# Kernel tuning notes

Measured on AMD Instinct MI355X. Metric: run time of the kernel, lower is better.

## Reference

```python
import jax, jax.numpy as jnp
import numpy as np

V, BLK, D, H, L = 32000, 2048, 768, 12, 2
HD = D // H

def _ln(x, g, b, eps=1e-5):
    m = jnp.mean(x, axis=-1, keepdims=True)
    v = jnp.var(x, axis=-1, keepdims=True)
    return (x - m) * jax.lax.rsqrt(v + eps) * g + b

def setup_inputs() -> dict:
    key = jax.random.key(0)
    ks = jax.random.split(key, 16)
    s = 0.02
    return {
        "idx": jax.random.randint(ks[0], (2, 2048), 0, V, dtype=jnp.int32),
        "wte": jax.random.normal(ks[1], (V, D), jnp.float32) * s,
        "wpe": jax.random.normal(ks[2], (BLK, D), jnp.float32) * s,
        "ln1_g": jnp.ones((L, D), jnp.float32),
        "ln1_b": jnp.zeros((L, D), jnp.float32),
        "qkv_w": jax.random.normal(ks[3], (L, 3 * D, D), jnp.float32) * s,
        "qkv_b": jnp.zeros((L, 3 * D), jnp.float32),
        "proj_w": jax.random.normal(ks[4], (L, D, D), jnp.float32) * s,
        "proj_b": jnp.zeros((L, D), jnp.float32),
        "ln2_g": jnp.ones((L, D), jnp.float32),
        "ln2_b": jnp.zeros((L, D), jnp.float32),
        "fc_w": jax.random.normal(ks[5], (L, 4 * D, D), jnp.float32) * s,
        "fc_b": jnp.zeros((L, 4 * D), jnp.float32),
        "fc2_w": jax.random.normal(ks[6], (L, D, 4 * D), jnp.float32) * s,
        "fc2_b": jnp.zeros((L, D), jnp.float32),
        "lnf_g": jnp.ones((D,), jnp.float32),
        "lnf_b": jnp.zeros((D,), jnp.float32),
    }

def reference(idx, wte, wpe, ln1_g, ln1_b, qkv_w, qkv_b, proj_w, proj_b,
              ln2_g, ln2_b, fc_w, fc_b, fc2_w, fc2_b, lnf_g, lnf_b):
    B, T = idx.shape
    x = wte[idx] + wpe[:T][None, :, :]  # [B,T,D]
    causal = jnp.tril(jnp.ones((T, T), dtype=bool))
    scale = 1.0 / np.sqrt(HD)
    for l in range(L):
        h = _ln(x, ln1_g[l], ln1_b[l])
        qkv = h @ qkv_w[l].T + qkv_b[l]               # [B,T,3D]
        q, k, v = jnp.split(qkv, 3, axis=-1)
        q = q.reshape(B, T, H, HD).transpose(0, 2, 1, 3)
        k = k.reshape(B, T, H, HD).transpose(0, 2, 1, 3)
        v = v.reshape(B, T, H, HD).transpose(0, 2, 1, 3)
        att = jnp.einsum('bhqd,bhkd->bhqk', q, k) * scale
        att = jnp.where(causal, att, -jnp.inf)
        att = jax.nn.softmax(att, axis=-1)
        y = jnp.einsum('bhqk,bhkd->bhqd', att, v)
        y = y.transpose(0, 2, 1, 3).reshape(B, T, D)
        x = x + y @ proj_w[l].T + proj_b[l]
        h = _ln(x, ln2_g[l], ln2_b[l])
        h = jax.nn.gelu(h @ fc_w[l].T + fc_b[l], approximate=False)
        x = x + h @ fc2_w[l].T + fc2_b[l]
    x = _ln(x, lnf_g, lnf_b)
    logits = x @ wte.T  # tied lm_head, [B,T,V]
    return logits
```

## Files before the change

kernel.cpp:

```cpp
#include <hip/hip_runtime.h>
#include <hip/hip_bf16.h>
#include <math.h>

#define BB 2
#define TT 2048
#define DD 768
#define HH 12
#define NTOK (BB*TT)
#define VV 32000
#define NL 2

typedef __hip_bfloat16 bf16;
typedef __attribute__((ext_vector_type(8))) short bf16x8;
typedef __attribute__((ext_vector_type(4))) float f32x4;

typedef const __attribute__((address_space(1))) unsigned int* gas_u32;
typedef __attribute__((address_space(3))) unsigned int* las_u32;

__device__ __forceinline__ void gload16(const bf16* g, bf16* l) {
    __builtin_amdgcn_global_load_lds((gas_u32)g, (las_u32)l, 16, 0, 0);
}

__global__ void cast_f2b(const float* __restrict__ in, bf16* __restrict__ out, int n4) {
    int i = blockIdx.x * 256 + threadIdx.x;
    if (i >= n4) return;
    float4 v = reinterpret_cast<const float4*>(in)[i];
    out[i*4+0] = __float2bfloat16(v.x);
    out[i*4+1] = __float2bfloat16(v.y);
    out[i*4+2] = __float2bfloat16(v.z);
    out[i*4+3] = __float2bfloat16(v.w);
}

__global__ void embed_k(const int* __restrict__ idx, const float* __restrict__ wte,
                        const float* __restrict__ wpe, float* __restrict__ x) {
    int i = blockIdx.x * 256 + threadIdx.x;
    int n = i / (DD/4), d4 = i - n * (DD/4);
    int tok = idx[n];
    int t = n & (TT - 1);
    float4 a = reinterpret_cast<const float4*>(wte + (size_t)tok * DD)[d4];
    float4 p = reinterpret_cast<const float4*>(wpe + (size_t)t * DD)[d4];
    float4 r; r.x = a.x+p.x; r.y = a.y+p.y; r.z = a.z+p.z; r.w = a.w+p.w;
    reinterpret_cast<float4*>(x)[i] = r;
}

__global__ __launch_bounds__(256) void ln_k(const float* __restrict__ x,
                                            const float* __restrict__ g,
                                            const float* __restrict__ b,
                                            bf16* __restrict__ out) {
    int row = blockIdx.x;
    int tid = threadIdx.x;
    const float* xr = x + (size_t)row * DD;
    float v0 = xr[tid], v1 = xr[tid + 256], v2 = xr[tid + 512];
    float s = v0 + v1 + v2;
    float ss = v0*v0 + v1*v1 + v2*v2;
    #pragma unroll
    for (int d = 1; d < 64; d <<= 1) { s += __shfl_xor(s, d, 64); ss += __shfl_xor(ss, d, 64); }
    __shared__ float sh[8];
    int w = tid >> 6;
    if ((tid & 63) == 0) { sh[w] = s; sh[4 + w] = ss; }
    __syncthreads();
    s  = sh[0] + sh[1] + sh[2] + sh[3];
    ss = sh[4] + sh[5] + sh[6] + sh[7];
    float mean = s * (1.0f / DD);
    float var  = ss * (1.0f / DD) - mean * mean;
    float rstd = rsqrtf(var + 1e-5f);
    bf16* orow = out + (size_t)row * DD;
    orow[tid]       = __float2bfloat16((v0 - mean) * rstd * g[tid]       + b[tid]);
    orow[tid + 256] = __float2bfloat16((v1 - mean) * rstd * g[tid + 256] + b[tid + 256]);
    orow[tid + 512] = __float2bfloat16((v2 - mean) * rstd * g[tid + 512] + b[tid + 512]);
}

template<int EPI, bool SWZ>
__global__ __launch_bounds__(512, 1) void gemm256(
    const bf16* __restrict__ A, const bf16* __restrict__ W,
    const float* __restrict__ bias, const float* __restrict__ resid,
    void* __restrict__ outp, int O, int K, int nwgx)
{
    __shared__ bf16 smem_bf[65536];
    char* smem = (char*)smem_bf;
    const int tid = threadIdx.x, lane = tid & 63, wid = tid >> 6;
    const int wm = wid >> 2, wn = wid & 3;
    int f = blockIdx.x;
    if (SWZ) { int x = f & 7, r = f >> 3; f = x * ((int)gridDim.x >> 3) + r; }
    const int by = f / nwgx;
    const int bx = f - by * nwgx;
    const int rowBase = by * 256, colBase = bx * 256;
    const int rr = lane & 15, s4 = lane >> 4;
    const int swz = (rr >> 1) & 3;
    const int aOff = (wm * 128 + rr) * 64 + ((s4 ^ swz) << 4);
    const int bOff = (wn * 64 + rr) * 64 + ((s4 ^ swz) << 4);
    const int st_r = (wid << 4) + (lane >> 2);
    const int st_j = lane & 3;
    const bf16* Asrc = A + (size_t)rowBase * K;
    const bf16* Wsrc = W + (size_t)colBase * K;
    const int nk = K >> 6;

    auto STAGE = [&](const bf16* src, int mat, int kt, int kk) {
        char* base = smem + ((kt & 1) << 16) + (mat << 15) + (kk << 14);
        #pragma unroll
        for (int L = 0; L < 2; ++L) {
            int r = (L << 7) + st_r;
            int gs = st_j ^ ((r >> 1) & 3);
            gload16(src + (size_t)r * K + (kt << 6) + (kk << 5) + (gs << 3),
                    (bf16*)(base + (L << 13) + (wid << 10)));
        }
    };

    f32x4 acc[8][4];
    #pragma unroll
    for (int m = 0; m < 8; ++m)
        #pragma unroll
        for (int n = 0; n < 4; ++n) acc[m][n] = (f32x4){0.f, 0.f, 0.f, 0.f};

    STAGE(Asrc, 0, 0, 0); STAGE(Wsrc, 1, 0, 0); STAGE(Asrc, 0, 0, 1); STAGE(Wsrc, 1, 0, 1);
    STAGE(Asrc, 0, 1, 0); STAGE(Wsrc, 1, 1, 0); STAGE(Asrc, 0, 1, 1);
    asm volatile("s_waitcnt vmcnt(6)" ::: "memory");
    __builtin_amdgcn_s_barrier();

    bf16x8 af[8], bfr[2];
    for (int kt = 0; kt < nk; ++kt) {
        char* Ab = smem + ((kt & 1) << 16);
        char* Bb = Ab + 32768;
        #pragma unroll
        for (int q = 0; q < 4; ++q) {
            const int kk = q >> 1, nh = q & 1;
            if (nh == 0) {
                #pragma unroll
                for (int m = 0; m < 8; ++m)
                    af[m] = *reinterpret_cast<const bf16x8*>(Ab + (kk << 14) + aOff + (m << 10));
            }
            bfr[0] = *reinterpret_cast<const bf16x8*>(Bb + (kk << 14) + bOff + ((nh * 2 + 0) << 10));
            bfr[1] = *reinterpret_cast<const bf16x8*>(Bb + (kk << 14) + bOff + ((nh * 2 + 1) << 10));
            if (q == 0) { if (kt + 1 < nk) STAGE(Wsrc, 1, kt + 1, 1); }
            else if (q == 1) { if (kt + 2 < nk) STAGE(Asrc, 0, kt + 2, 0); }
            else if (q == 2) { if (kt + 2 < nk) STAGE(Wsrc, 1, kt + 2, 0); }
            else { if (kt + 2 < nk) STAGE(Asrc, 0, kt + 2, 1); }
            __builtin_amdgcn_s_barrier();
            __builtin_amdgcn_s_setprio(1);
            #pragma unroll
            for (int m = 0; m < 8; ++m) {
                acc[m][nh * 2 + 0] = __builtin_amdgcn_mfma_f32_16x16x32_bf16(af[m], bfr[0], acc[m][nh * 2 + 0], 0, 0, 0);
                acc[m][nh * 2 + 1] = __builtin_amdgcn_mfma_f32_16x16x32_bf16(af[m], bfr[1], acc[m][nh * 2 + 1], 0, 0, 0);
            }
            __builtin_amdgcn_s_setprio(0);
            if (q == 3) asm volatile("s_waitcnt vmcnt(6)" ::: "memory");
            __builtin_amdgcn_s_barrier();
        }
    }

    #pragma unroll
    for (int m = 0; m < 8; ++m) {
        int row = rowBase + wm * 128 + m * 16 + s4 * 4;
        #pragma unroll
        for (int n = 0; n < 4; ++n) {
            int col = colBase + wn * 64 + n * 16 + rr;
            float bv = bias ? bias[col] : 0.f;
            #pragma unroll
            for (int j2 = 0; j2 < 4; ++j2) {
                float v = acc[m][n][j2] + bv;
                size_t oi = (size_t)(row + j2) * O + col;
                if (EPI == 1) v += resid[oi];
                if (EPI == 2) {
                    v = 0.5f * v * (1.0f + erff(v * 0.70710678118654752f));
                    reinterpret_cast<bf16*>(outp)[oi] = __float2bfloat16(v);
                } else if (EPI == 3) {
                    reinterpret_cast<bf16*>(outp)[oi] = __float2bfloat16(v);
                } else {
                    reinterpret_cast<float*>(outp)[oi] = v;
                }
            }
        }
    }
}

template<int EPI>
__global__ __launch_bounds__(256) void gemm_bt(
    const bf16* __restrict__ A, const bf16* __restrict__ W,
    const float* __restrict__ bias, const float* __restrict__ resid,
    void* __restrict__ outp, int O, int K)
{
    __shared__ bf16 As[128 * 32];
    __shared__ bf16 Bs[128 * 32];
    const int tid = threadIdx.x;
    const int lane = tid & 63;
    const int w = tid >> 6;
    const int wm = w >> 1, wn = w & 1;
    const int rowBase = blockIdx.y * 128, colBase = blockIdx.x * 128;

    const int rr = lane & 15, kq = (lane >> 4) * 8;
    const int srow = lane >> 2;
    const int scol = (lane & 3) * 8;

    f32x4 acc[4][4];
    #pragma unroll
    for (int m = 0; m < 4; ++m)
        #pragma unroll
        for (int n = 0; n < 4; ++n) acc[m][n] = (f32x4){0.f, 0.f, 0.f, 0.f};

    for (int k0 = 0; k0 < K; k0 += 32) {
        #pragma unroll
        for (int p = 0; p < 2; ++p) {
            int s = w * 16 + p * 64;
            gload16(&A[(size_t)(rowBase + s + srow) * K + k0 + scol], &As[s * 32]);
            gload16(&W[(size_t)(colBase + s + srow) * K + k0 + scol], &Bs[s * 32]);
        }
        __syncthreads();
        bf16x8 a[4], b[4];
        #pragma unroll
        for (int m = 0; m < 4; ++m)
            a[m] = *reinterpret_cast<const bf16x8*>(&As[(wm * 64 + m * 16 + rr) * 32 + kq]);
        #pragma unroll
        for (int n = 0; n < 4; ++n)
            b[n] = *reinterpret_cast<const bf16x8*>(&Bs[(wn * 64 + n * 16 + rr) * 32 + kq]);
        #pragma unroll
        for (int m = 0; m < 4; ++m)
            #pragma unroll
            for (int n = 0; n < 4; ++n)
                acc[m][n] = __builtin_amdgcn_mfma_f32_16x16x32_bf16(a[m], b[n], acc[m][n], 0, 0, 0);
        __syncthreads();
    }

    #pragma unroll
    for (int m = 0; m < 4; ++m) {
        int row = rowBase + wm * 64 + m * 16 + (lane >> 4) * 4;
        #pragma unroll
        for (int n = 0; n < 4; ++n) {
            int col = colBase + wn * 64 + n * 16 + (lane & 15);
            float bv = bias ? bias[col] : 0.f;
            #pragma unroll
            for (int j2 = 0; j2 < 4; ++j2) {
                float v = acc[m][n][j2] + bv;
                size_t oi = (size_t)(row + j2) * O + col;
                if (EPI == 1) v += resid[oi];
                if (EPI == 2) {
                    v = 0.5f * v * (1.0f + erff(v * 0.70710678118654752f));
                    reinterpret_cast<bf16*>(outp)[oi] = __float2bfloat16(v);
                } else if (EPI == 3) {
                    reinterpret_cast<bf16*>(outp)[oi] = __float2bfloat16(v);
                } else {
                    reinterpret_cast<float*>(outp)[oi] = v;
                }
            }
        }
    }
}

__global__ __launch_bounds__(256, 2) void attn_flash(const bf16* __restrict__ qkvb,
                                                     bf16* __restrict__ ybf)
{
    __shared__ bf16 Qs[128][72];
    __shared__ bf16 Ks[64][72];
    __shared__ bf16 Vt[64][72];

    const int tid = threadIdx.x, lane = tid & 63, w = tid >> 6;
    const int qi = 15 - (blockIdx.x / 24);
    const int bh = blockIdx.x % 24;
    const int b = bh / HH, h = bh % HH;
    const int qbase = qi * 128;
    const int rr = lane & 15, g8 = (lane >> 4) * 8, g4 = (lane >> 4) * 4;

    {
        int seg = tid & 7, jr = tid >> 3;
        #pragma unroll
        for (int p = 0; p < 4; ++p) {
            int q = jr + p * 32;
            *reinterpret_cast<uint4*>(&Qs[q][seg * 8]) =
                *reinterpret_cast<const uint4*>(&qkvb[(size_t)(b*TT + qbase + q) * 2304 + h*64 + seg*8]);
        }
    }
    __syncthreads();

    bf16x8 qf[2][2];
    #pragma unroll
    for (int m = 0; m < 2; ++m)
        #pragma unroll
        for (int c = 0; c < 2; ++c)
            qf[m][c] = *reinterpret_cast<const bf16x8*>(&Qs[w*32 + m*16 + rr][c*32 + g8]);

    float mst[2][4], lst[2][4];
    f32x4 o[2][4];
    #pragma unroll
    for (int m = 0; m < 2; ++m)
        #pragma unroll
        for (int jj = 0; jj < 4; ++jj) { mst[m][jj] = -1e30f; lst[m][jj] = 0.f; }
    #pragma unroll
    for (int m = 0; m < 2; ++m)
        #pragma unroll
        for (int nd = 0; nd < 4; ++nd) o[m][nd] = (f32x4){0.f,0.f,0.f,0.f};

    const int ktmax = 2 * qi + 2;
    for (int kt = 0; kt < ktmax; ++kt) {
        __syncthreads();
        {
            int seg = tid & 7, jr = tid >> 3;
            #pragma unroll
            for (int p = 0; p < 2; ++p) {
                int j = jr + p * 32;
                *reinterpret_cast<uint4*>(&Ks[j][seg * 8]) =
                    *reinterpret_cast<const uint4*>(&qkvb[(size_t)(b*TT + kt*64 + j) * 2304 + DD + h*64 + seg*8]);
            }
            int jv = tid & 31, d0 = (tid >> 5) * 8;
            #pragma unroll
            for (int p = 0; p < 2; ++p) {
                int j = jv + p * 32;
                uint4 raw = *reinterpret_cast<const uint4*>(&qkvb[(size_t)(b*TT + kt*64 + j) * 2304 + 2*DD + h*64 + d0]);
                const bf16* vv = reinterpret_cast<const bf16*>(&raw);
                #pragma unroll
                for (int i2 = 0; i2 < 8; ++i2) Vt[d0 + i2][j] = vv[i2];
            }
        }
        __syncthreads();

        bf16x8 kf[4][2];
        #pragma unroll
        for (int n = 0; n < 4; ++n)
            #pragma unroll
            for (int c = 0; c < 2; ++c)
                kf[n][c] = *reinterpret_cast<const bf16x8*>(&Ks[n*16 + rr][c*32 + g8]);
        f32x4 sacc[2][4];
        #pragma unroll
        for (int m = 0; m < 2; ++m)
            #pragma unroll
            for (int n = 0; n < 4; ++n) sacc[m][n] = (f32x4){0.f,0.f,0.f,0.f};
        #pragma unroll
        for (int m = 0; m < 2; ++m)
            #pragma unroll
            for (int n = 0; n < 4; ++n)
                #pragma unroll
                for (int c = 0; c < 2; ++c)
                    sacc[m][n] = __builtin_amdgcn_mfma_f32_16x16x32_bf16(qf[m][c], kf[n][c], sacc[m][n], 0, 0, 0);

        float corr[2][4];
        #pragma unroll
        for (int m = 0; m < 2; ++m) {
            #pragma unroll
            for (int jj = 0; jj < 4; ++jj) {
                const int qg = qbase + w*32 + m*16 + g4 + jj;
                float pm = -1e30f;
                #pragma unroll
                for (int n = 0; n < 4; ++n) {
                    float v = sacc[m][n][jj] * 0.125f;
                    int jg = kt*64 + n*16 + rr;
                    v = (jg <= qg) ? v : -1e30f;
                    sacc[m][n][jj] = v;
                    pm = fmaxf(pm, v);
                }
                pm = fmaxf(pm, __shfl_xor(pm, 1, 64));
                pm = fmaxf(pm, __shfl_xor(pm, 2, 64));
                pm = fmaxf(pm, __shfl_xor(pm, 4, 64));
                pm = fmaxf(pm, __shfl_xor(pm, 8, 64));
                float nm = fmaxf(mst[m][jj], pm);
                float cv = __expf(mst[m][jj] - nm);
                float r = 0.f;
                #pragma unroll
                for (int n = 0; n < 4; ++n) {
                    float p = __expf(sacc[m][n][jj] - nm);
                    r += p;
                    Qs[w*32 + m*16 + g4 + jj][n*16 + rr] = __float2bfloat16(p);
                }
                r += __shfl_xor(r, 1, 64);
                r += __shfl_xor(r, 2, 64);
                r += __shfl_xor(r, 4, 64);
                r += __shfl_xor(r, 8, 64);
                lst[m][jj] = lst[m][jj] * cv + r;
                mst[m][jj] = nm;
                corr[m][jj] = cv;
            }
        }
        #pragma unroll
        for (int m = 0; m < 2; ++m)
            #pragma unroll
            for (int nd = 0; nd < 4; ++nd)
                #pragma unroll
                for (int jj = 0; jj < 4; ++jj) o[m][nd][jj] *= corr[m][jj];

        __builtin_amdgcn_sched_barrier(0);

        bf16x8 pf[2][2], vf[4][2];
        #pragma unroll
        for (int m = 0; m < 2; ++m)
            #pragma unroll
            for (int c = 0; c < 2; ++c)
                pf[m][c] = *reinterpret_cast<const bf16x8*>(&Qs[w*32 + m*16 + rr][c*32 + g8]);
        #pragma unroll
        for (int nd = 0; nd < 4; ++nd)
            #pragma unroll
            for (int c = 0; c < 2; ++c)
                vf[nd][c] = *reinterpret_cast<const bf16x8*>(&Vt[nd*16 + rr][c*32 + g8]);
        #pragma unroll
        for (int m = 0; m < 2; ++m)
            #pragma unroll
            for (int nd = 0; nd < 4; ++nd)
                #pragma unroll
                for (int c = 0; c < 2; ++c)
                    o[m][nd] = __builtin_amdgcn_mfma_f32_16x16x32_bf16(pf[m][c], vf[nd][c], o[m][nd], 0, 0, 0);
    }

    #pragma unroll
    for (int m = 0; m < 2; ++m) {
        #pragma unroll
        for (int jj = 0; jj < 4; ++jj) {
            const int qg = qbase + w*32 + m*16 + g4 + jj;
            const float inv = 1.0f / lst[m][jj];
            #pragma unroll
            for (int nd = 0; nd < 4; ++nd)
                ybf[(size_t)(b*TT + qg) * DD + h*64 + nd*16 + rr] =
                    __float2bfloat16(o[m][nd][jj] * inv);
        }
    }
}

extern "C" void kernel_launch(void* const* d_in, const int* in_sizes, int n_in,
                              void* d_out, int out_size, void* d_ws, size_t ws_size,
                              hipStream_t stream) {
    const int*   idx    = (const int*)  d_in[0];
    const float* wte    = (const float*)d_in[1];
    const float* wpe    = (const float*)d_in[2];
    const float* ln1_g  = (const float*)d_in[3];
    const float* ln1_b  = (const float*)d_in[4];
    const float* qkv_w  = (const float*)d_in[5];
    const float* qkv_b  = (const float*)d_in[6];
    const float* proj_w = (const float*)d_in[7];
    const float* proj_b = (const float*)d_in[8];
    const float* ln2_g  = (const float*)d_in[9];
    const float* ln2_b  = (const float*)d_in[10];
    const float* fc_w   = (const float*)d_in[11];
    const float* fc_b   = (const float*)d_in[12];
    const float* fc2_w  = (const float*)d_in[13];
    const float* fc2_b  = (const float*)d_in[14];
    const float* lnf_g  = (const float*)d_in[15];
    const float* lnf_b  = (const float*)d_in[16];

    char* ws = (char*)d_ws;
    size_t off = 0;
    auto alloc = [&](size_t bytes) -> void* {
        void* p = ws + off;
        off += (bytes + 255) & ~(size_t)255;
        return p;
    };
    float* x     = (float*)alloc((size_t)NTOK * DD * 4);
    bf16*  qkvb  = (bf16*) alloc((size_t)NTOK * 3 * DD * 2);
    bf16*  lnb   = (bf16*) alloc((size_t)NTOK * DD * 2);
    bf16*  ybf   = (bf16*) alloc((size_t)NTOK * DD * 2);
    bf16*  ffb   = (bf16*) alloc((size_t)NTOK * 4 * DD * 2);
    bf16*  w_qkv = (bf16*) alloc((size_t)NL * 3 * DD * DD * 2);
    bf16*  w_prj = (bf16*) alloc((size_t)NL * DD * DD * 2);
    bf16*  w_fc  = (bf16*) alloc((size_t)NL * 4 * DD * DD * 2);
    bf16*  w_fc2 = (bf16*) alloc((size_t)NL * DD * 4 * DD * 2);
    bf16*  w_wte = (bf16*) alloc((size_t)VV * DD * 2);

    auto conv = [&](const float* src, bf16* dst, size_t n) {
        int n4 = (int)(n / 4);
        cast_f2b<<<dim3((n4 + 255) / 256), dim3(256), 0, stream>>>(src, dst, n4);
    };
    conv(wte,    w_wte, (size_t)VV * DD);
    conv(qkv_w,  w_qkv, (size_t)NL * 3 * DD * DD);
    conv(proj_w, w_prj, (size_t)NL * DD * DD);
    conv(fc_w,   w_fc,  (size_t)NL * 4 * DD * DD);
    conv(fc2_w,  w_fc2, (size_t)NL * DD * 4 * DD);

    embed_k<<<dim3(NTOK * (DD/4) / 256), dim3(256), 0, stream>>>(idx, wte, wpe, x);

    for (int l = 0; l < NL; ++l) {
        ln_k<<<dim3(NTOK), dim3(256), 0, stream>>>(x, ln1_g + l * DD, ln1_b + l * DD, lnb);
        gemm_bt<3><<<dim3(3 * DD / 128, 32), dim3(256), 0, stream>>>(
            lnb, w_qkv + (size_t)l * 3 * DD * DD, qkv_b + l * 3 * DD, nullptr,
            (void*)qkvb, 3 * DD, DD);
        attn_flash<<<dim3(24 * (TT / 128)), dim3(256), 0, stream>>>(qkvb, ybf);
        gemm_bt<1><<<dim3(DD / 128, 32), dim3(256), 0, stream>>>(
            ybf, w_prj + (size_t)l * DD * DD, proj_b + l * DD, x,
            (void*)x, DD, DD);
        ln_k<<<dim3(NTOK), dim3(256), 0, stream>>>(x, ln2_g + l * DD, ln2_b + l * DD, lnb);
        gemm_bt<2><<<dim3(4 * DD / 128, 32), dim3(256), 0, stream>>>(
            lnb, w_fc + (size_t)l * 4 * DD * DD, fc_b + l * 4 * DD, nullptr,
            (void*)ffb, 4 * DD, DD);
        gemm_bt<1><<<dim3(DD / 128, 32), dim3(256), 0, stream>>>(
            ffb, w_fc2 + (size_t)l * DD * 4 * DD, fc2_b + l * DD, x,
            (void*)x, DD, 4 * DD);
    }

    ln_k<<<dim3(NTOK), dim3(256), 0, stream>>>(x, lnf_g, lnf_b, lnb);
    gemm256<0, true><<<dim3((VV / 256) * (NTOK / 256)), dim3(512), 0, stream>>>(
        lnb, w_wte, nullptr, nullptr, d_out, VV, DD, VV / 256);
}
```

Before: 884.2 us.

## Prefetch next K/V tile into registers in attention, skip masks, remap lm_head tiles

The flash attention loop now loads the next K/V tile from global memory into registers while the current tile is being computed, and stores it to LDS at the start of the next iteration. This hides global load latency behind the MFMA work. Causal masking is skipped for sub-tiles that lie entirely below the diagonal, and s_setprio is raised around the MFMA blocks. The lm_head GEMM also switches to a new block-to-tile mapping that groups 16 row tiles across 8 XCD-strided slots, which changes cache locality.

```diff
diff --git a/kernel.cpp b/kernel.cpp
--- a/kernel.cpp
+++ b/kernel.cpp
@@ -70,7 +70,7 @@
     orow[tid + 512] = __float2bfloat16((v2 - mean) * rstd * g[tid + 512] + b[tid + 512]);
 }
 
-template<int EPI, bool SWZ>
+template<int EPI, int SWZMODE>
 __global__ __launch_bounds__(512, 1) void gemm256(
     const bf16* __restrict__ A, const bf16* __restrict__ W,
     const float* __restrict__ bias, const float* __restrict__ resid,
@@ -81,9 +81,14 @@
     const int tid = threadIdx.x, lane = tid & 63, wid = tid >> 6;
     const int wm = wid >> 2, wn = wid & 3;
     int f = blockIdx.x;
-    if (SWZ) { int x = f & 7, r = f >> 3; f = x * ((int)gridDim.x >> 3) + r; }
-    const int by = f / nwgx;
-    const int bx = f - by * nwgx;
+    int by, bx;
+    if (SWZMODE == 2) {
+        int x = f & 7, r = f >> 3;
+        by = x * 2 + (r & 1);
+        bx = r >> 1;
+    } else {
+        by = f / nwgx; bx = f - by * nwgx;
+    }
     const int rowBase = by * 256, colBase = bx * 256;
     const int rr = lane & 15, s4 = lane >> 4;
     const int swz = (rr >> 1) & 3;
@@ -268,6 +273,20 @@
                 *reinterpret_cast<const uint4*>(&qkvb[(size_t)(b*TT + qbase + q) * 2304 + h*64 + seg*8]);
         }
     }
+
+    const int seg = tid & 7, jr = tid >> 3;
+    const int jv = tid & 31, d0 = (tid >> 5) * 8;
+    const bf16* kbase = qkvb + (size_t)b * TT * 2304 + DD + h * 64;
+    const bf16* vbase = qkvb + (size_t)b * TT * 2304 + 2 * DD + h * 64;
+    uint4 kreg[2], vreg[2];
+    auto LOADKV = [&](int kt) {
+        #pragma unroll
+        for (int p = 0; p < 2; ++p) {
+            kreg[p] = *reinterpret_cast<const uint4*>(&kbase[(size_t)(kt*64 + jr + p*32) * 2304 + seg*8]);
+            vreg[p] = *reinterpret_cast<const uint4*>(&vbase[(size_t)(kt*64 + jv + p*32) * 2304 + d0]);
+        }
+    };
+    LOADKV(0);
     __syncthreads();
 
     bf16x8 qf[2][2];
@@ -290,26 +309,17 @@
 
     const int ktmax = 2 * qi + 2;
     for (int kt = 0; kt < ktmax; ++kt) {
-        __syncthreads();
-        {
-            int seg = tid & 7, jr = tid >> 3;
-            #pragma unroll
-            for (int p = 0; p < 2; ++p) {
-                int j = jr + p * 32;
-                *reinterpret_cast<uint4*>(&Ks[j][seg * 8]) =
-                    *reinterpret_cast<const uint4*>(&qkvb[(size_t)(b*TT + kt*64 + j) * 2304 + DD + h*64 + seg*8]);
-            }
-            int jv = tid & 31, d0 = (tid >> 5) * 8;
-            #pragma unroll
-            for (int p = 0; p < 2; ++p) {
-                int j = jv + p * 32;
-                uint4 raw = *reinterpret_cast<const uint4*>(&qkvb[(size_t)(b*TT + kt*64 + j) * 2304 + 2*DD + h*64 + d0]);
-                const bf16* vv = reinterpret_cast<const bf16*>(&raw);
-                #pragma unroll
-                for (int i2 = 0; i2 < 8; ++i2) Vt[d0 + i2][j] = vv[i2];
-            }
-        }
-        __syncthreads();
+        #pragma unroll
+        for (int p = 0; p < 2; ++p) {
+            *reinterpret_cast<uint4*>(&Ks[jr + p*32][seg*8]) = kreg[p];
+            const bf16* vv = reinterpret_cast<const bf16*>(&vreg[p]);
+            #pragma unroll
+            for (int i2 = 0; i2 < 8; ++i2) Vt[d0 + i2][jv + p*32] = vv[i2];
+        }
+        if (kt + 1 < ktmax) LOADKV(kt + 1);
+        asm volatile("s_waitcnt lgkmcnt(0)" ::: "memory");
+        __builtin_amdgcn_s_barrier();
+        __builtin_amdgcn_sched_barrier(0);
 
         bf16x8 kf[4][2];
         #pragma unroll
@@ -322,6 +332,7 @@
         for (int m = 0; m < 2; ++m)
             #pragma unroll
             for (int n = 0; n < 4; ++n) sacc[m][n] = (f32x4){0.f,0.f,0.f,0.f};
+        __builtin_amdgcn_s_setprio(1);
         #pragma unroll
         for (int m = 0; m < 2; ++m)
             #pragma unroll
@@ -329,10 +340,12 @@
                 #pragma unroll
                 for (int c = 0; c < 2; ++c)
                     sacc[m][n] = __builtin_amdgcn_mfma_f32_16x16x32_bf16(qf[m][c], kf[n][c], sacc[m][n], 0, 0, 0);
+        __builtin_amdgcn_s_setprio(0);
 
         float corr[2][4];
         #pragma unroll
         for (int m = 0; m < 2; ++m) {
+            const bool needMask = (kt*64 + 63) > (qbase + w*32 + m*16);
             #pragma unroll
             for (int jj = 0; jj < 4; ++jj) {
                 const int qg = qbase + w*32 + m*16 + g4 + jj;
@@ -340,8 +353,10 @@
                 #pragma unroll
                 for (int n = 0; n < 4; ++n) {
                     float v = sacc[m][n][jj] * 0.125f;
-                    int jg = kt*64 + n*16 + rr;
-                    v = (jg <= qg) ? v : -1e30f;
+                    if (needMask) {
+                        int jg = kt*64 + n*16 + rr;
+                        v = (jg <= qg) ? v : -1e30f;
+                    }
                     sacc[m][n][jj] = v;
                     pm = fmaxf(pm, v);
                 }
@@ -387,6 +402,7 @@
             #pragma unroll
             for (int c = 0; c < 2; ++c)
                 vf[nd][c] = *reinterpret_cast<const bf16x8*>(&Vt[nd*16 + rr][c*32 + g8]);
+        __builtin_amdgcn_s_setprio(1);
         #pragma unroll
         for (int m = 0; m < 2; ++m)
             #pragma unroll
@@ -394,6 +410,9 @@
                 #pragma unroll
                 for (int c = 0; c < 2; ++c)
                     o[m][nd] = __builtin_amdgcn_mfma_f32_16x16x32_bf16(pf[m][c], vf[nd][c], o[m][nd], 0, 0, 0);
+        __builtin_amdgcn_s_setprio(0);
+
+        __builtin_amdgcn_s_barrier();
     }
 
     #pragma unroll
@@ -480,6 +499,6 @@
     }
 
     ln_k<<<dim3(NTOK), dim3(256), 0, stream>>>(x, lnf_g, lnf_b, lnb);
-    gemm256<0, true><<<dim3((VV / 256) * (NTOK / 256)), dim3(512), 0, stream>>>(
+    gemm256<0, 2><<<dim3((VV / 256) * (NTOK / 256)), dim3(512), 0, stream>>>(
         lnb, w_wte, nullptr, nullptr, d_out, VV, DD, VV / 256);
 }
```

New measurement: 917.0 us. +3.7%, slower.

## Fold softmax scale into Q, use exp2, skip rescale and masking when unneeded

Applied to the files above, without the earlier changes.

Pre-multiplies Q by scale·log2(e) so the softmax can use exp2f without a per-element scale. It skips causal masking on KV tiles that are fully below the diagonal. It also skips the running-max update and output rescale when the new row max exceeds the old one by at most 8 in log2 units (lazy rescaling). MFMA sections are wrapped in s_setprio to favour matrix issue. The risks are bf16 rounding of the pre-scaled Q and the possibility that lazy rescaling lets values grow up to 2^8 before normalisation. The GEMM swizzle template parameter is renamed without changing behaviour.

```diff
diff --git a/kernel.cpp b/kernel.cpp
--- a/kernel.cpp
+++ b/kernel.cpp
@@ -19,6 +19,13 @@
 
 __device__ __forceinline__ void gload16(const bf16* g, bf16* l) {
     __builtin_amdgcn_global_load_lds((gas_u32)g, (las_u32)l, 16, 0, 0);
+}
+__device__ __forceinline__ float b2f(short s) {
+    union { float f; unsigned u; } x; x.u = ((unsigned)(unsigned short)s) << 16; return x.f;
+}
+__device__ __forceinline__ short f2b(float f) {
+    __hip_bfloat16 h = __float2bfloat16(f);
+    return *reinterpret_cast<short*>(&h);
 }
 
 __global__ void cast_f2b(const float* __restrict__ in, bf16* __restrict__ out, int n4) {
@@ -70,7 +77,7 @@
     orow[tid + 512] = __float2bfloat16((v2 - mean) * rstd * g[tid + 512] + b[tid + 512]);
 }
 
-template<int EPI, bool SWZ>
+template<int EPI, int SWZMODE>
 __global__ __launch_bounds__(512, 1) void gemm256(
     const bf16* __restrict__ A, const bf16* __restrict__ W,
     const float* __restrict__ bias, const float* __restrict__ resid,
@@ -81,7 +88,7 @@
     const int tid = threadIdx.x, lane = tid & 63, wid = tid >> 6;
     const int wm = wid >> 2, wn = wid & 3;
     int f = blockIdx.x;
-    if (SWZ) { int x = f & 7, r = f >> 3; f = x * ((int)gridDim.x >> 3) + r; }
+    if (SWZMODE == 1) { int x = f & 7, r = f >> 3; f = x * ((int)gridDim.x >> 3) + r; }
     const int by = f / nwgx;
     const int bx = f - by * nwgx;
     const int rowBase = by * 256, colBase = bx * 256;
@@ -274,8 +281,12 @@
     #pragma unroll
     for (int m = 0; m < 2; ++m)
         #pragma unroll
-        for (int c = 0; c < 2; ++c)
-            qf[m][c] = *reinterpret_cast<const bf16x8*>(&Qs[w*32 + m*16 + rr][c*32 + g8]);
+        for (int c = 0; c < 2; ++c) {
+            bf16x8 v = *reinterpret_cast<const bf16x8*>(&Qs[w*32 + m*16 + rr][c*32 + g8]);
+            #pragma unroll
+            for (int e = 0; e < 8; ++e) v[e] = f2b(b2f(v[e]) * 0.180336880111f);
+            qf[m][c] = v;
+        }
 
     float mst[2][4], lst[2][4];
     f32x4 o[2][4];
@@ -322,6 +333,7 @@
         for (int m = 0; m < 2; ++m)
             #pragma unroll
             for (int n = 0; n < 4; ++n) sacc[m][n] = (f32x4){0.f,0.f,0.f,0.f};
+        __builtin_amdgcn_s_setprio(1);
         #pragma unroll
         for (int m = 0; m < 2; ++m)
             #pragma unroll
@@ -329,50 +341,85 @@
                 #pragma unroll
                 for (int c = 0; c < 2; ++c)
                     sacc[m][n] = __builtin_amdgcn_mfma_f32_16x16x32_bf16(qf[m][c], kf[n][c], sacc[m][n], 0, 0, 0);
-
-        float corr[2][4];
+        __builtin_amdgcn_s_setprio(0);
+
+        float pm[2][4];
+        float need = -1e30f;
         #pragma unroll
         for (int m = 0; m < 2; ++m) {
+            const bool needMask = (kt*64 + 63) > (qbase + w*32 + m*16);
             #pragma unroll
             for (int jj = 0; jj < 4; ++jj) {
                 const int qg = qbase + w*32 + m*16 + g4 + jj;
-                float pm = -1e30f;
+                float pv = -1e30f;
                 #pragma unroll
                 for (int n = 0; n < 4; ++n) {
-                    float v = sacc[m][n][jj] * 0.125f;
-                    int jg = kt*64 + n*16 + rr;
-                    v = (jg <= qg) ? v : -1e30f;
-                    sacc[m][n][jj] = v;
-                    pm = fmaxf(pm, v);
+                    float v = sacc[m][n][jj];
+                    if (needMask) {
+                        int jg = kt*64 + n*16 + rr;
+                        v = (jg <= qg) ? v : -1e30f;
+                        sacc[m][n][jj] = v;
+                    }
+                    pv = fmaxf(pv, v);
                 }
-                pm = fmaxf(pm, __shfl_xor(pm, 1, 64));
-                pm = fmaxf(pm, __shfl_xor(pm, 2, 64));
-                pm = fmaxf(pm, __shfl_xor(pm, 4, 64));
-                pm = fmaxf(pm, __shfl_xor(pm, 8, 64));
-                float nm = fmaxf(mst[m][jj], pm);
-                float cv = __expf(mst[m][jj] - nm);
-                float r = 0.f;
-                #pragma unroll
-                for (int n = 0; n < 4; ++n) {
-                    float p = __expf(sacc[m][n][jj] - nm);
-                    r += p;
-                    Qs[w*32 + m*16 + g4 + jj][n*16 + rr] = __float2bfloat16(p);
+                pv = fmaxf(pv, __shfl_xor(pv, 1, 64));
+                pv = fmaxf(pv, __shfl_xor(pv, 2, 64));
+                pv = fmaxf(pv, __shfl_xor(pv, 4, 64));
+                pv = fmaxf(pv, __shfl_xor(pv, 8, 64));
+                pm[m][jj] = pv;
+                need = fmaxf(need, pv - mst[m][jj]);
+            }
+        }
+
+        if (__all(need <= 8.0f)) {
+            #pragma unroll
+            for (int m = 0; m < 2; ++m)
+                #pragma unroll
+                for (int jj = 0; jj < 4; ++jj) {
+                    const float mm = mst[m][jj];
+                    float r = 0.f;
+                    #pragma unroll
+                    for (int n = 0; n < 4; ++n) {
+                        float p = exp2f(sacc[m][n][jj] - mm);
+                        r += p;
+                        Qs[w*32 + m*16 + g4 + jj][n*16 + rr] = __float2bfloat16(p);
+                    }
+                    r += __shfl_xor(r, 1, 64);
+                    r += __shfl_xor(r, 2, 64);
+                    r += __shfl_xor(r, 4, 64);
+                    r += __shfl_xor(r, 8, 64);
+                    lst[m][jj] += r;
                 }
-                r += __shfl_xor(r, 1, 64);
-                r += __shfl_xor(r, 2, 64);
-                r += __shfl_xor(r, 4, 64);
-                r += __shfl_xor(r, 8, 64);
-                lst[m][jj] = lst[m][jj] * cv + r;
-                mst[m][jj] = nm;
-                corr[m][jj] = cv;
-            }
-        }
-        #pragma unroll
-        for (int m = 0; m < 2; ++m)
-            #pragma unroll
-            for (int nd = 0; nd < 4; ++nd)
-                #pragma unroll
-                for (int jj = 0; jj < 4; ++jj) o[m][nd][jj] *= corr[m][jj];
+        } else {
+            float corr[2][4];
+            #pragma unroll
+            for (int m = 0; m < 2; ++m)
+                #pragma unroll
+                for (int jj = 0; jj < 4; ++jj) {
+                    float nm = fmaxf(mst[m][jj], pm[m][jj]);
+                    float cv = exp2f(mst[m][jj] - nm);
+                    float r = 0.f;
+                    #pragma unroll
+                    for (int n = 0; n < 4; ++n) {
+                        float p = exp2f(sacc[m][n][jj] - nm);
+                        r += p;
+                        Qs[w*32 + m*16 + g4 + jj][n*16 + rr] = __float2bfloat16(p);
+                    }
+                    r += __shfl_xor(r, 1, 64);
+                    r += __shfl_xor(r, 2, 64);
+                    r += __shfl_xor(r, 4, 64);
+                    r += __shfl_xor(r, 8, 64);
+                    lst[m][jj] = lst[m][jj] * cv + r;
+                    mst[m][jj] = nm;
+                    corr[m][jj] = cv;
+                }
+            #pragma unroll
+            for (int m = 0; m < 2; ++m)
+                #pragma unroll
+                for (int nd = 0; nd < 4; ++nd)
+                    #pragma unroll
+                    for (int jj = 0; jj < 4; ++jj) o[m][nd][jj] *= corr[m][jj];
+        }
 
         __builtin_amdgcn_sched_barrier(0);
 
@@ -387,6 +434,7 @@
             #pragma unroll
             for (int c = 0; c < 2; ++c)
                 vf[nd][c] = *reinterpret_cast<const bf16x8*>(&Vt[nd*16 + rr][c*32 + g8]);
+        __builtin_amdgcn_s_setprio(1);
         #pragma unroll
         for (int m = 0; m < 2; ++m)
             #pragma unroll
@@ -394,6 +442,7 @@
                 #pragma unroll
                 for (int c = 0; c < 2; ++c)
                     o[m][nd] = __builtin_amdgcn_mfma_f32_16x16x32_bf16(pf[m][c], vf[nd][c], o[m][nd], 0, 0, 0);
+        __builtin_amdgcn_s_setprio(0);
     }
 
     #pragma unroll
@@ -480,6 +529,6 @@
     }
 
     ln_k<<<dim3(NTOK), dim3(256), 0, stream>>>(x, lnf_g, lnf_b, lnb);
-    gemm256<0, true><<<dim3((VV / 256) * (NTOK / 256)), dim3(512), 0, stream>>>(
+    gemm256<0, 1><<<dim3((VV / 256) * (NTOK / 256)), dim3(512), 0, stream>>>(
         lnb, w_wte, nullptr, nullptr, d_out, VV, DD, VV / 256);
 }
```

Result: slower. 915.3 us (+3.5%).
